# Kernel tuning notes

Measured on AMD Instinct MI355X. Metric: run time of the kernel, lower is better.

## Reference

```python
import jax, jax.numpy as jnp
import numpy as np

N = 50000        # nodes
E = 800000       # edges
H = 128          # hidden_channels
NH = 4           # num_heads
HD = H // NH     # head_dim
EPS = 1e-5       # LayerNorm eps (torch default)


def setup_inputs() -> dict:
    key = jax.random.key(0)
    ks = jax.random.split(key, 16)
    s = 0.02
    return {
        "x": jax.random.normal(ks[0], (N, H), dtype=jnp.float32),
        "edge_index": jax.random.randint(ks[1], (2, E), 0, N, dtype=jnp.int64),
        "Wq": jax.random.normal(ks[2], (H, H), dtype=jnp.float32) * s,
        "bq": jnp.zeros((H,), jnp.float32),
        "Wk": jax.random.normal(ks[3], (H, H), dtype=jnp.float32) * s,
        "bk": jnp.zeros((H,), jnp.float32),
        "Wv": jax.random.normal(ks[4], (H, H), dtype=jnp.float32) * s,
        "bv": jnp.zeros((H,), jnp.float32),
        "W1": jax.random.normal(ks[5], (2 * H, H), dtype=jnp.float32) * s,
        "b1": jnp.zeros((H,), jnp.float32),
        "ln_g": jnp.ones((H,), jnp.float32),
        "ln_b": jnp.zeros((H,), jnp.float32),
        "W2": jax.random.normal(ks[6], (H, H), dtype=jnp.float32) * s,
        "b2": jnp.zeros((H,), jnp.float32),
    }


def reference(x, edge_index, Wq, bq, Wk, bk, Wv, bv, W1, b1, ln_g, ln_b, W2, b2):
    n = x.shape[0]
    row, col = edge_index[0], edge_index[1]
    # dense projections, split heads: [N, NH, HD]
    Q = (x @ Wq + bq).reshape(n, NH, HD)
    K = (x @ Wk + bk).reshape(n, NH, HD)
    V = (x @ Wv + bv).reshape(n, NH, HD)
    # edge-wise gather + per-head dot product: [E, NH]
    scores = (Q[row] * K[col]).sum(-1) / jnp.sqrt(jnp.float32(HD))
    # segment softmax over edges grouped by destination node (row)
    m = jax.ops.segment_max(scores, row, num_segments=n)        # [N, NH]
    m = jnp.where(jnp.isfinite(m), m, 0.0)                      # empty segments -> 0
    e = jnp.exp(scores - m[row])                                # [E, NH]
    denom = jax.ops.segment_sum(e, row, num_segments=n)         # [N, NH]
    w = e / denom[row]                                          # [E, NH]
    # weighted scatter-add aggregation: [N, H]
    msg = (w[..., None] * V[col]).reshape(-1, NH * HD)          # [E, H]
    agg = jax.ops.segment_sum(msg, row, num_segments=n)         # [N, H]
    # MLP: Linear -> ReLU -> LayerNorm -> Linear, plus residual
    h = jax.nn.relu(jnp.concatenate([x, agg], axis=-1) @ W1 + b1)
    mu = h.mean(-1, keepdims=True)
    var = ((h - mu) ** 2).mean(-1, keepdims=True)
    h = (h - mu) / jnp.sqrt(var + EPS) * ln_g + ln_b
    return h @ W2 + b2 + x
```

## Files before the change

kernel.cpp:

```cpp
#include <hip/hip_runtime.h>
#include <hip/hip_bf16.h>

#define NN 50000
#define HH 128
#define NHEAD 4
#define HD 32
#define EE 800000
#define LN_EPS 1e-5f
#define ROWS_PAD 50048
#define SCAN_NB 98

typedef __bf16 bf16x8 __attribute__((ext_vector_type(8)));
typedef short  s16x8  __attribute__((ext_vector_type(8)));
typedef float  f32x4  __attribute__((ext_vector_type(4)));

__device__ __forceinline__ f32x4 mfma_bf16(s16x8 a, s16x8 b, f32x4 c) {
    return __builtin_amdgcn_mfma_f32_16x16x32_bf16((bf16x8)a, (bf16x8)b, c, 0, 0, 0);
}

__device__ __forceinline__ unsigned short f2bf(float f) {
    union { float f; unsigned int u; } v; v.f = f;
    unsigned int u = v.u + 0x7FFFu + ((v.u >> 16) & 1u);
    return (unsigned short)(u >> 16);
}
__device__ __forceinline__ float bf2f(unsigned short h) {
    union { unsigned int u; float f; } v; v.u = ((unsigned int)h) << 16;
    return v.f;
}
__device__ __forceinline__ float bflo(unsigned int w) { return __uint_as_float(w << 16); }
__device__ __forceinline__ float bfhi(unsigned int w) { return __uint_as_float(w & 0xffff0000u); }

__global__ void detect_idx_kernel(const unsigned int* __restrict__ buf, int* __restrict__ flag) {
    if (blockIdx.x == 0 && threadIdx.x == 0) {
        int is64 = 1;
        for (int i = 0; i < 64; ++i) {
            if (buf[2 * i + 1] != 0u) { is64 = 0; break; }
        }
        *flag = is64;
    }
}

__global__ void convert_hist_kernel(const void* __restrict__ ei, const int* __restrict__ flag,
                                    int* __restrict__ rowi, int* __restrict__ coli,
                                    int* __restrict__ deg) {
    int i = (blockIdx.x * blockDim.x + threadIdx.x) * 2;
    if (i >= EE) return;
    int r0, r1, c0, c1;
    if (*flag) {
        const longlong2* pr = (const longlong2*)((const long long*)ei + i);
        const longlong2* pc = (const longlong2*)((const long long*)ei + EE + i);
        longlong2 rv = *pr, cv = *pc;
        r0 = (int)rv.x; r1 = (int)rv.y;
        c0 = (int)cv.x; c1 = (int)cv.y;
    } else {
        const int2* pr = (const int2*)((const int*)ei + i);
        const int2* pc = (const int2*)((const int*)ei + EE + i);
        int2 rv = *pr, cv = *pc;
        r0 = rv.x; r1 = rv.y;
        c0 = cv.x; c1 = cv.y;
    }
    *(int2*)(rowi + i) = make_int2(r0, r1);
    *(int2*)(coli + i) = make_int2(c0, c1);
    atomicAdd(&deg[r0], 1);
    atomicAdd(&deg[r1], 1);
}

__global__ __launch_bounds__(512) void scan_a_kernel(const int* __restrict__ deg,
                                                     int* __restrict__ bsum) {
    __shared__ int red[8];
    const int t = threadIdx.x;
    const int gid = blockIdx.x * 512 + t;
    int v = (gid < NN) ? deg[gid] : 0;
    #pragma unroll
    for (int o = 1; o < 64; o <<= 1) v += __shfl_xor(v, o);
    if ((t & 63) == 0) red[t >> 6] = v;
    __syncthreads();
    if (t == 0) {
        int s = 0;
        #pragma unroll
        for (int k = 0; k < 8; ++k) s += red[k];
        bsum[blockIdx.x] = s;
    }
}

__global__ void scan_b_kernel(const int* __restrict__ bsum, int* __restrict__ boff) {
    const int lane = threadIdx.x;
    const int i0 = lane * 2, i1 = lane * 2 + 1;
    int a = (i0 < SCAN_NB) ? bsum[i0] : 0;
    int b = (i1 < SCAN_NB) ? bsum[i1] : 0;
    int incl = a + b;
    const int own = incl;
    #pragma unroll
    for (int o = 1; o < 64; o <<= 1) {
        int u = __shfl_up(incl, o);
        if (lane >= o) incl += u;
    }
    int excl = incl - own;
    if (i0 < SCAN_NB) boff[i0] = excl;
    if (i1 < SCAN_NB) boff[i1] = excl + a;
}

__global__ __launch_bounds__(512) void scan_c_kernel(const int* __restrict__ deg,
                                                     const int* __restrict__ boff,
                                                     int* __restrict__ rstart,
                                                     int* __restrict__ cursor) {
    __shared__ int wsum[8];
    const int t = threadIdx.x;
    const int gid = blockIdx.x * 512 + t;
    const int lane = t & 63, w = t >> 6;
    int v = (gid < NN) ? deg[gid] : 0;
    int incl = v;
    #pragma unroll
    for (int o = 1; o < 64; o <<= 1) {
        int u = __shfl_up(incl, o);
        if (lane >= o) incl += u;
    }
    if (lane == 63) wsum[w] = incl;
    __syncthreads();
    int woff = 0;
    for (int k = 0; k < w; ++k) woff += wsum[k];
    int excl = boff[blockIdx.x] + woff + incl - v;
    if (gid < NN) { rstart[gid] = excl; cursor[gid] = excl; }
    if (gid == 0) rstart[NN] = EE;
}

__global__ void scatter_kernel(const int* __restrict__ rowi, const int* __restrict__ coli,
                               int* __restrict__ cursor, int* __restrict__ colS) {
    int i = blockIdx.x * blockDim.x + threadIdx.x;
    if (i >= EE) return;
    int pos = atomicAdd(&cursor[rowi[i]], 1);
    colS[pos] = coli[i];
}

__global__ void pack_w_kernel(const float* __restrict__ Wq, const float* __restrict__ Wk,
                              const float* __restrict__ Wv, const float* __restrict__ W1,
                              const float* __restrict__ W2, unsigned short* __restrict__ wf) {
    int i = blockIdx.x * blockDim.x + threadIdx.x;
    if (i >= 98304) return;
    float val;
    if (i < 49152) {
        int j = i & 7, lane = (i >> 3) & 63, kk = (i >> 9) & 3, nt = i >> 11;
        int k = kk * 32 + (lane >> 4) * 8 + j;
        int n = nt * 16 + (lane & 15);
        const float* W = (n < 128) ? Wq : ((n < 256) ? Wk : Wv);
        val = W[k * HH + (n & 127)];
    } else if (i < 81920) {
        int local = i - 49152;
        int j = local & 7, lane = (local >> 3) & 63, kk = (local >> 9) & 7, nt = local >> 12;
        int k = kk * 32 + (lane >> 4) * 8 + j;
        int n = nt * 16 + (lane & 15);
        val = W1[k * HH + n];
    } else {
        int local = i - 81920;
        int j = local & 7, lane = (local >> 3) & 63, kk = (local >> 9) & 3, nt = local >> 11;
        int k = kk * 32 + (lane >> 4) * 8 + j;
        int n = nt * 16 + (lane & 15);
        val = W2[k * HH + n];
    }
    wf[i] = f2bf(val);
}

__global__ __launch_bounds__(256) void qkvx_kernel(
        const float* __restrict__ x, const unsigned short* __restrict__ wf,
        const float* __restrict__ bq, const float* __restrict__ bk, const float* __restrict__ bv,
        unsigned short* __restrict__ xa,
        unsigned short* __restrict__ Qb, unsigned short* __restrict__ Kb,
        unsigned short* __restrict__ Vb) {
    const int wave = threadIdx.x >> 6, lane = threadIdx.x & 63;
    const int row0 = blockIdx.x * 64 + wave * 16;
    const int arow = row0 + (lane & 15);
    const int kbase = (lane >> 4) * 8;

    s16x8 a[4];
    if (arow < NN) {
        const float* xp = x + (size_t)arow * HH + kbase;
        #pragma unroll
        for (int kk = 0; kk < 4; ++kk) {
            float4 f0 = *(const float4*)(xp + kk * 32);
            float4 f1 = *(const float4*)(xp + kk * 32 + 4);
            s16x8 av;
            av[0] = (short)f2bf(f0.x); av[1] = (short)f2bf(f0.y);
            av[2] = (short)f2bf(f0.z); av[3] = (short)f2bf(f0.w);
            av[4] = (short)f2bf(f1.x); av[5] = (short)f2bf(f1.y);
            av[6] = (short)f2bf(f1.z); av[7] = (short)f2bf(f1.w);
            a[kk] = av;
            *(s16x8*)(xa + (size_t)arow * 256 + kbase + kk * 32) = av;
        }
    } else {
        #pragma unroll
        for (int kk = 0; kk < 4; ++kk) a[kk] = (s16x8)0;
    }

    f32x4 acc[24];
    #pragma unroll
    for (int nt = 0; nt < 24; ++nt) acc[nt] = (f32x4){0.f, 0.f, 0.f, 0.f};

    const s16x8* wfv = (const s16x8*)wf;
    #pragma unroll
    for (int nt = 0; nt < 24; ++nt) {
        #pragma unroll
        for (int kk = 0; kk < 4; ++kk) {
            s16x8 b = wfv[(nt * 4 + kk) * 64 + lane];
            acc[nt] = mfma_bf16(a[kk], b, acc[nt]);
        }
    }

    const int colb = lane & 15;
    const int rbase = row0 + (lane >> 4) * 4;
    #pragma unroll
    for (int nt = 0; nt < 24; ++nt) {
        const int mtx = nt >> 3;
        const int nc = (nt & 7) * 16 + colb;
        const float* bias_p = (mtx == 0) ? bq : ((mtx == 1) ? bk : bv);
        unsigned short* O = (mtx == 0) ? Qb : ((mtx == 1) ? Kb : Vb);
        float bias = bias_p[nc];
        #pragma unroll
        for (int r = 0; r < 4; ++r)
            O[(size_t)(rbase + r) * 128 + nc] = f2bf(acc[nt][r] + bias);
    }
}

__global__ __launch_bounds__(256) void attn_kernel(
        const unsigned short* __restrict__ Qb, const unsigned short* __restrict__ Kb,
        const unsigned short* __restrict__ Vb, const int* __restrict__ rstart,
        const int* __restrict__ colS, unsigned short* __restrict__ xa) {
    const int wave = threadIdx.x >> 6;
    const int lane = threadIdx.x & 63;
    const int i = blockIdx.x * 4 + wave;
    if (i >= NN) return;
    const int h = lane & 3;
    const int le = lane >> 2;
    const int half = lane >> 5;
    const int sl = lane & 31;
    const int g2 = sl >> 3;
    const int e0 = rstart[i], e1 = rstart[i + 1];
    const int deg = e1 - e0;

    float qf[32];
    {
        const uint4* qp = (const uint4*)(Qb + (size_t)i * 128 + h * 32);
        #pragma unroll
        for (int cch = 0; cch < 4; ++cch) {
            uint4 qv = qp[cch];
            unsigned int w_[4] = {qv.x, qv.y, qv.z, qv.w};
            #pragma unroll
            for (int dd = 0; dd < 4; ++dd) {
                qf[cch * 8 + dd * 2]     = bflo(w_[dd]);
                qf[cch * 8 + dd * 2 + 1] = bfhi(w_[dd]);
            }
        }
    }

    float m = -INFINITY, l = 0.f;
    float acc0 = 0.f, acc1 = 0.f, acc2 = 0.f, acc3 = 0.f;

    for (int c0 = 0; c0 < deg; c0 += 16) {
        const int cnt = min(16, deg - c0);
        int col = 0;
        float s = -INFINITY;
        if (le < cnt) {
            col = colS[e0 + c0 + le];
            const uint4* kp = (const uint4*)(Kb + (size_t)col * 128 + h * 32);
            float dot = 0.f;
            #pragma unroll
            for (int cch = 0; cch < 4; ++cch) {
                uint4 kv = kp[cch];
                unsigned int w_[4] = {kv.x, kv.y, kv.z, kv.w};
                #pragma unroll
                for (int dd = 0; dd < 4; ++dd) {
                    dot += qf[cch * 8 + dd * 2]     * bflo(w_[dd]);
                    dot += qf[cch * 8 + dd * 2 + 1] * bfhi(w_[dd]);
                }
            }
            s = dot * 0.17677669529663689f;
        }
        float sm = s;
        sm = fmaxf(sm, __shfl_xor(sm, 4));
        sm = fmaxf(sm, __shfl_xor(sm, 8));
        sm = fmaxf(sm, __shfl_xor(sm, 16));
        sm = fmaxf(sm, __shfl_xor(sm, 32));
        const float mn = fmaxf(m, sm);
        const float p = (le < cnt) ? __expf(s - mn) : 0.f;
        float ps = p;
        ps += __shfl_xor(ps, 4);
        ps += __shfl_xor(ps, 8);
        ps += __shfl_xor(ps, 16);
        ps += __shfl_xor(ps, 32);
        const float fac = __expf(m - mn);
        l = l * fac + ps;
        m = mn;
        const float facbc = __shfl(fac, g2);
        acc0 *= facbc; acc1 *= facbc; acc2 *= facbc; acc3 *= facbc;
        #pragma unroll
        for (int e2 = 0; e2 < 8; ++e2) {
            const int e = 2 * e2 + half;
            const int   cbc = __shfl(col, 4 * e);
            const float pbc = __shfl(p, 4 * e + g2);
            const uint2 v2 = *(const uint2*)(Vb + (size_t)cbc * 128 + 4 * sl);
            acc0 += pbc * bflo(v2.x);
            acc1 += pbc * bfhi(v2.x);
            acc2 += pbc * bflo(v2.y);
            acc3 += pbc * bfhi(v2.y);
        }
    }

    acc0 += __shfl_xor(acc0, 32);
    acc1 += __shfl_xor(acc1, 32);
    acc2 += __shfl_xor(acc2, 32);
    acc3 += __shfl_xor(acc3, 32);
    const float lf = __shfl(l, g2);
    const float rinv = (lf > 0.f) ? 1.f / lf : 0.f;
    if (half == 0) {
        uint2 o;
        o.x = ((unsigned int)f2bf(acc1 * rinv) << 16) | (unsigned int)f2bf(acc0 * rinv);
        o.y = ((unsigned int)f2bf(acc3 * rinv) << 16) | (unsigned int)f2bf(acc2 * rinv);
        *(uint2*)(xa + (size_t)i * 256 + 128 + 4 * sl) = o;
    }
}

__global__ __launch_bounds__(256) void gemm_mlp1_kernel(
        const unsigned short* __restrict__ xa, const unsigned short* __restrict__ w1f,
        const float* __restrict__ b1, const float* __restrict__ ln_g,
        const float* __restrict__ ln_b, unsigned short* __restrict__ hb) {
    const int wave = threadIdx.x >> 6, lane = threadIdx.x & 63;
    const int row0 = blockIdx.x * 64 + wave * 16;
    const int arow = row0 + (lane & 15);

    s16x8 a[8];
    const unsigned short* ap = xa + (size_t)arow * 256 + (lane >> 4) * 8;
    #pragma unroll
    for (int kk = 0; kk < 8; ++kk) a[kk] = *(const s16x8*)(ap + kk * 32);

    f32x4 acc[8];
    #pragma unroll
    for (int nt = 0; nt < 8; ++nt) acc[nt] = (f32x4){0.f, 0.f, 0.f, 0.f};

    const s16x8* wfv = (const s16x8*)w1f;
    #pragma unroll
    for (int nt = 0; nt < 8; ++nt) {
        #pragma unroll
        for (int kk = 0; kk < 8; ++kk) {
            s16x8 b = wfv[(nt * 8 + kk) * 64 + lane];
            acc[nt] = mfma_bf16(a[kk], b, acc[nt]);
        }
    }

    const int colb = lane & 15;
    #pragma unroll
    for (int nt = 0; nt < 8; ++nt) {
        float bias = b1[nt * 16 + colb];
        #pragma unroll
        for (int r = 0; r < 4; ++r) {
            float v = acc[nt][r] + bias;
            acc[nt][r] = v > 0.f ? v : 0.f;
        }
    }
    float mu[4], rs[4];
    #pragma unroll
    for (int r = 0; r < 4; ++r) {
        float s = 0.f, q = 0.f;
        #pragma unroll
        for (int nt = 0; nt < 8; ++nt) { float v = acc[nt][r]; s += v; q += v * v; }
        #pragma unroll
        for (int msk = 1; msk < 16; msk <<= 1) {
            s += __shfl_xor(s, msk, 16);
            q += __shfl_xor(q, msk, 16);
        }
        float m_ = s * (1.f / 128.f);
        float var = q * (1.f / 128.f) - m_ * m_;
        mu[r] = m_;
        rs[r] = rsqrtf(var + LN_EPS);
    }
    const int rbase = row0 + (lane >> 4) * 4;
    #pragma unroll
    for (int nt = 0; nt < 8; ++nt) {
        int col = nt * 16 + colb;
        float g = ln_g[col], bb = ln_b[col];
        #pragma unroll
        for (int r = 0; r < 4; ++r) {
            float h = (acc[nt][r] - mu[r]) * rs[r] * g + bb;
            hb[(size_t)(rbase + r) * 128 + col] = f2bf(h);
        }
    }
}

__global__ __launch_bounds__(256) void gemm_mlp2_kernel(
        const unsigned short* __restrict__ hb, const unsigned short* __restrict__ w2f,
        const float* __restrict__ b2, const unsigned short* __restrict__ xa,
        float* __restrict__ out) {
    const int wave = threadIdx.x >> 6, lane = threadIdx.x & 63;
    const int row0 = blockIdx.x * 64 + wave * 16;
    const int arow = row0 + (lane & 15);

    s16x8 a[4];
    const unsigned short* ap = hb + (size_t)arow * 128 + (lane >> 4) * 8;
    #pragma unroll
    for (int kk = 0; kk < 4; ++kk) a[kk] = *(const s16x8*)(ap + kk * 32);

    f32x4 acc[8];
    #pragma unroll
    for (int nt = 0; nt < 8; ++nt) acc[nt] = (f32x4){0.f, 0.f, 0.f, 0.f};

    const s16x8* wfv = (const s16x8*)w2f;
    #pragma unroll
    for (int nt = 0; nt < 8; ++nt) {
        #pragma unroll
        for (int kk = 0; kk < 4; ++kk) {
            s16x8 b = wfv[(nt * 4 + kk) * 64 + lane];
            acc[nt] = mfma_bf16(a[kk], b, acc[nt]);
        }
    }

    const int colb = lane & 15;
    const int rbase = row0 + (lane >> 4) * 4;
    #pragma unroll
    for (int nt = 0; nt < 8; ++nt) {
        int col = nt * 16 + colb;
        float bias = b2[col];
        #pragma unroll
        for (int r = 0; r < 4; ++r) {
            int row = rbase + r;
            if (row < NN)
                out[(size_t)row * 128 + col] =
                    acc[nt][r] + bias + bf2f(xa[(size_t)row * 256 + col]);
        }
    }
}

extern "C" void kernel_launch(void* const* d_in, const int* in_sizes, int n_in,
                              void* d_out, int out_size, void* d_ws, size_t ws_size,
                              hipStream_t stream) {
    const float* x    = (const float*)d_in[0];
    const void*  ei   = d_in[1];
    const float* Wq   = (const float*)d_in[2];
    const float* bq   = (const float*)d_in[3];
    const float* Wk   = (const float*)d_in[4];
    const float* bk   = (const float*)d_in[5];
    const float* Wv   = (const float*)d_in[6];
    const float* bv   = (const float*)d_in[7];
    const float* W1   = (const float*)d_in[8];
    const float* b1   = (const float*)d_in[9];
    const float* ln_g = (const float*)d_in[10];
    const float* ln_b = (const float*)d_in[11];
    const float* W2   = (const float*)d_in[12];
    const float* b2   = (const float*)d_in[13];
    float* out = (float*)d_out;

    char* ws = (char*)d_ws;
    size_t off = 0;
    auto alloc = [&](size_t bytes) {
        size_t o = off;
        off = (off + bytes + 255) & ~(size_t)255;
        return o;
    };
    size_t flag_o = alloc(sizeof(int));
    size_t rowi_o = alloc((size_t)EE * sizeof(int));
    size_t coli_o = alloc((size_t)EE * sizeof(int));
    size_t deg_o  = alloc((size_t)NN * sizeof(int));
    size_t cur_o  = alloc((size_t)NN * sizeof(int));
    size_t rs_o   = alloc((size_t)(NN + 1) * sizeof(int));
    size_t bsum_o = alloc((size_t)SCAN_NB * sizeof(int));
    size_t boff_o = alloc((size_t)SCAN_NB * sizeof(int));
    size_t colS_o = alloc((size_t)EE * sizeof(int));
    size_t xa_o   = alloc((size_t)ROWS_PAD * 256 * sizeof(unsigned short));
    size_t wf_o   = alloc((size_t)98304 * sizeof(unsigned short));
    size_t Qb_o   = alloc((size_t)ROWS_PAD * 128 * sizeof(unsigned short));
    size_t Kb_o   = alloc((size_t)ROWS_PAD * 128 * sizeof(unsigned short));
    size_t Vb_o   = alloc((size_t)ROWS_PAD * 128 * sizeof(unsigned short));
    size_t hb_o   = Qb_o;

    int* flag   = (int*)(ws + flag_o);
    int* rowi   = (int*)(ws + rowi_o);
    int* coli   = (int*)(ws + coli_o);
    int* deg    = (int*)(ws + deg_o);
    int* cursor = (int*)(ws + cur_o);
    int* rstart = (int*)(ws + rs_o);
    int* bsum   = (int*)(ws + bsum_o);
    int* boff   = (int*)(ws + boff_o);
    int* colS   = (int*)(ws + colS_o);
    unsigned short* xa = (unsigned short*)(ws + xa_o);
    unsigned short* wf = (unsigned short*)(ws + wf_o);
    unsigned short* Qb = (unsigned short*)(ws + Qb_o);
    unsigned short* Kb = (unsigned short*)(ws + Kb_o);
    unsigned short* Vb = (unsigned short*)(ws + Vb_o);
    unsigned short* hb = (unsigned short*)(ws + hb_o);

    hipMemsetAsync(ws + deg_o, 0, (size_t)NN * sizeof(int), stream);

    detect_idx_kernel<<<1, 64, 0, stream>>>((const unsigned int*)ei, flag);
    convert_hist_kernel<<<(EE / 2 + 255) / 256, 256, 0, stream>>>(ei, flag, rowi, coli, deg);
    scan_a_kernel<<<SCAN_NB, 512, 0, stream>>>(deg, bsum);
    scan_b_kernel<<<1, 64, 0, stream>>>(bsum, boff);
    scan_c_kernel<<<SCAN_NB, 512, 0, stream>>>(deg, boff, rstart, cursor);
    scatter_kernel<<<(EE + 255) / 256, 256, 0, stream>>>(rowi, coli, cursor, colS);

    pack_w_kernel<<<98304 / 256, 256, 0, stream>>>(Wq, Wk, Wv, W1, W2, wf);

    qkvx_kernel<<<ROWS_PAD / 64, 256, 0, stream>>>(x, wf, bq, bk, bv, xa, Qb, Kb, Vb);

    attn_kernel<<<(NN + 3) / 4, 256, 0, stream>>>(Qb, Kb, Vb, rstart, colS, xa);

    gemm_mlp1_kernel<<<ROWS_PAD / 64, 256, 0, stream>>>(xa, wf + 49152, b1, ln_g, ln_b, hb);

    gemm_mlp2_kernel<<<ROWS_PAD / 64, 256, 0, stream>>>(hb, wf + 81920, b2, xa, out);
}
```

Before: 224.1 us.

## Build CSR via atomic ranks, fold block-offset scan, batch four nodes per attention wave

The histogram kernel now records each edge's atomic rank within its row, so the scatter writes colS at rstart[row]+rank with no second round of atomics. The rowi/coli copies and the cursor array go away, and edge_index is re-read directly. The separate block-offset scan kernel is dropped; each scan_c block sums the preceding block totals itself. The attention kernel processes four nodes per wave sequentially, which cuts the block count, but it now relies on NN being divisible by 16 and loses latency hiding from a larger grid.

Measured after the change: 193.8 us. 1.16x faster.

```diff
diff --git a/kernel.cpp b/kernel.cpp
--- a/kernel.cpp
+++ b/kernel.cpp
@@ -40,29 +40,21 @@
     }
 }
 
-__global__ void convert_hist_kernel(const void* __restrict__ ei, const int* __restrict__ flag,
-                                    int* __restrict__ rowi, int* __restrict__ coli,
-                                    int* __restrict__ deg) {
+__global__ void hist_kernel(const void* __restrict__ ei, const int* __restrict__ flag,
+                            int* __restrict__ deg, int* __restrict__ rank) {
     int i = (blockIdx.x * blockDim.x + threadIdx.x) * 2;
     if (i >= EE) return;
-    int r0, r1, c0, c1;
+    int r0, r1;
     if (*flag) {
-        const longlong2* pr = (const longlong2*)((const long long*)ei + i);
-        const longlong2* pc = (const longlong2*)((const long long*)ei + EE + i);
-        longlong2 rv = *pr, cv = *pc;
+        longlong2 rv = *(const longlong2*)((const long long*)ei + i);
         r0 = (int)rv.x; r1 = (int)rv.y;
-        c0 = (int)cv.x; c1 = (int)cv.y;
     } else {
-        const int2* pr = (const int2*)((const int*)ei + i);
-        const int2* pc = (const int2*)((const int*)ei + EE + i);
-        int2 rv = *pr, cv = *pc;
+        int2 rv = *(const int2*)((const int*)ei + i);
         r0 = rv.x; r1 = rv.y;
-        c0 = cv.x; c1 = cv.y;
-    }
-    *(int2*)(rowi + i) = make_int2(r0, r1);
-    *(int2*)(coli + i) = make_int2(c0, c1);
-    atomicAdd(&deg[r0], 1);
-    atomicAdd(&deg[r1], 1);
+    }
+    int ra = atomicAdd(&deg[r0], 1);
+    int rb = atomicAdd(&deg[r1], 1);
+    *(int2*)(rank + i) = make_int2(ra, rb);
 }
 
 __global__ __launch_bounds__(512) void scan_a_kernel(const int* __restrict__ deg,
@@ -83,31 +75,21 @@
     }
 }
 
-__global__ void scan_b_kernel(const int* __restrict__ bsum, int* __restrict__ boff) {
-    const int lane = threadIdx.x;
-    const int i0 = lane * 2, i1 = lane * 2 + 1;
-    int a = (i0 < SCAN_NB) ? bsum[i0] : 0;
-    int b = (i1 < SCAN_NB) ? bsum[i1] : 0;
-    int incl = a + b;
-    const int own = incl;
-    #pragma unroll
-    for (int o = 1; o < 64; o <<= 1) {
-        int u = __shfl_up(incl, o);
-        if (lane >= o) incl += u;
-    }
-    int excl = incl - own;
-    if (i0 < SCAN_NB) boff[i0] = excl;
-    if (i1 < SCAN_NB) boff[i1] = excl + a;
-}
-
 __global__ __launch_bounds__(512) void scan_c_kernel(const int* __restrict__ deg,
-                                                     const int* __restrict__ boff,
-                                                     int* __restrict__ rstart,
-                                                     int* __restrict__ cursor) {
+                                                     const int* __restrict__ bsum,
+                                                     int* __restrict__ rstart) {
     __shared__ int wsum[8];
+    __shared__ int blockoff;
     const int t = threadIdx.x;
     const int gid = blockIdx.x * 512 + t;
     const int lane = t & 63, w = t >> 6;
+    if (t < 64) {
+        int s = 0;
+        for (int k = t; k < blockIdx.x; k += 64) s += bsum[k];
+        #pragma unroll
+        for (int o = 1; o < 64; o <<= 1) s += __shfl_xor(s, o);
+        if (t == 0) blockoff = s;
+    }
     int v = (gid < NN) ? deg[gid] : 0;
     int incl = v;
     #pragma unroll
@@ -119,17 +101,31 @@
     __syncthreads();
     int woff = 0;
     for (int k = 0; k < w; ++k) woff += wsum[k];
-    int excl = boff[blockIdx.x] + woff + incl - v;
-    if (gid < NN) { rstart[gid] = excl; cursor[gid] = excl; }
+    int excl = blockoff + woff + incl - v;
+    if (gid < NN) rstart[gid] = excl;
     if (gid == 0) rstart[NN] = EE;
 }
 
-__global__ void scatter_kernel(const int* __restrict__ rowi, const int* __restrict__ coli,
-                               int* __restrict__ cursor, int* __restrict__ colS) {
-    int i = blockIdx.x * blockDim.x + threadIdx.x;
+__global__ void scatter_kernel(const void* __restrict__ ei, const int* __restrict__ flag,
+                               const int* __restrict__ rank, const int* __restrict__ rstart,
+                               int* __restrict__ colS) {
+    int i = (blockIdx.x * blockDim.x + threadIdx.x) * 2;
     if (i >= EE) return;
-    int pos = atomicAdd(&cursor[rowi[i]], 1);
-    colS[pos] = coli[i];
+    int r0, r1, c0, c1;
+    if (*flag) {
+        longlong2 rv = *(const longlong2*)((const long long*)ei + i);
+        longlong2 cv = *(const longlong2*)((const long long*)ei + EE + i);
+        r0 = (int)rv.x; r1 = (int)rv.y;
+        c0 = (int)cv.x; c1 = (int)cv.y;
+    } else {
+        int2 rv = *(const int2*)((const int*)ei + i);
+        int2 cv = *(const int2*)((const int*)ei + EE + i);
+        r0 = rv.x; r1 = rv.y;
+        c0 = cv.x; c1 = cv.y;
+    }
+    int2 rk = *(const int2*)(rank + i);
+    colS[rstart[r0] + rk.x] = c0;
+    colS[rstart[r1] + rk.y] = c1;
 }
 
 __global__ void pack_w_kernel(const float* __restrict__ Wq, const float* __restrict__ Wk,
@@ -226,95 +222,98 @@
         const int* __restrict__ colS, unsigned short* __restrict__ xa) {
     const int wave = threadIdx.x >> 6;
     const int lane = threadIdx.x & 63;
-    const int i = blockIdx.x * 4 + wave;
-    if (i >= NN) return;
     const int h = lane & 3;
     const int le = lane >> 2;
     const int half = lane >> 5;
     const int sl = lane & 31;
     const int g2 = sl >> 3;
-    const int e0 = rstart[i], e1 = rstart[i + 1];
-    const int deg = e1 - e0;
-
-    float qf[32];
-    {
-        const uint4* qp = (const uint4*)(Qb + (size_t)i * 128 + h * 32);
-        #pragma unroll
-        for (int cch = 0; cch < 4; ++cch) {
-            uint4 qv = qp[cch];
-            unsigned int w_[4] = {qv.x, qv.y, qv.z, qv.w};
-            #pragma unroll
-            for (int dd = 0; dd < 4; ++dd) {
-                qf[cch * 8 + dd * 2]     = bflo(w_[dd]);
-                qf[cch * 8 + dd * 2 + 1] = bfhi(w_[dd]);
-            }
-        }
-    }
-
-    float m = -INFINITY, l = 0.f;
-    float acc0 = 0.f, acc1 = 0.f, acc2 = 0.f, acc3 = 0.f;
-
-    for (int c0 = 0; c0 < deg; c0 += 16) {
-        const int cnt = min(16, deg - c0);
-        int col = 0;
-        float s = -INFINITY;
-        if (le < cnt) {
-            col = colS[e0 + c0 + le];
-            const uint4* kp = (const uint4*)(Kb + (size_t)col * 128 + h * 32);
-            float dot = 0.f;
+    const int ibase = blockIdx.x * 16 + wave * 4;
+
+    for (int j = 0; j < 4; ++j) {
+        const int i = ibase + j;
+        const int e0 = rstart[i], e1 = rstart[i + 1];
+        const int deg = e1 - e0;
+
+        float qf[32];
+        {
+            const uint4* qp = (const uint4*)(Qb + (size_t)i * 128 + h * 32);
             #pragma unroll
             for (int cch = 0; cch < 4; ++cch) {
-                uint4 kv = kp[cch];
-                unsigned int w_[4] = {kv.x, kv.y, kv.z, kv.w};
+                uint4 qv = qp[cch];
+                unsigned int w_[4] = {qv.x, qv.y, qv.z, qv.w};
                 #pragma unroll
                 for (int dd = 0; dd < 4; ++dd) {
-                    dot += qf[cch * 8 + dd * 2]     * bflo(w_[dd]);
-                    dot += qf[cch * 8 + dd * 2 + 1] * bfhi(w_[dd]);
+                    qf[cch * 8 + dd * 2]     = bflo(w_[dd]);
+                    qf[cch * 8 + dd * 2 + 1] = bfhi(w_[dd]);
                 }
             }
-            s = dot * 0.17677669529663689f;
-        }
-        float sm = s;
-        sm = fmaxf(sm, __shfl_xor(sm, 4));
-        sm = fmaxf(sm, __shfl_xor(sm, 8));
-        sm = fmaxf(sm, __shfl_xor(sm, 16));
-        sm = fmaxf(sm, __shfl_xor(sm, 32));
-        const float mn = fmaxf(m, sm);
-        const float p = (le < cnt) ? __expf(s - mn) : 0.f;
-        float ps = p;
-        ps += __shfl_xor(ps, 4);
-        ps += __shfl_xor(ps, 8);
-        ps += __shfl_xor(ps, 16);
-        ps += __shfl_xor(ps, 32);
-        const float fac = __expf(m - mn);
-        l = l * fac + ps;
-        m = mn;
-        const float facbc = __shfl(fac, g2);
-        acc0 *= facbc; acc1 *= facbc; acc2 *= facbc; acc3 *= facbc;
-        #pragma unroll
-        for (int e2 = 0; e2 < 8; ++e2) {
-            const int e = 2 * e2 + half;
-            const int   cbc = __shfl(col, 4 * e);
-            const float pbc = __shfl(p, 4 * e + g2);
-            const uint2 v2 = *(const uint2*)(Vb + (size_t)cbc * 128 + 4 * sl);
-            acc0 += pbc * bflo(v2.x);
-            acc1 += pbc * bfhi(v2.x);
-            acc2 += pbc * bflo(v2.y);
-            acc3 += pbc * bfhi(v2.y);
-        }
-    }
-
-    acc0 += __shfl_xor(acc0, 32);
-    acc1 += __shfl_xor(acc1, 32);
-    acc2 += __shfl_xor(acc2, 32);
-    acc3 += __shfl_xor(acc3, 32);
-    const float lf = __shfl(l, g2);
-    const float rinv = (lf > 0.f) ? 1.f / lf : 0.f;
-    if (half == 0) {
-        uint2 o;
-        o.x = ((unsigned int)f2bf(acc1 * rinv) << 16) | (unsigned int)f2bf(acc0 * rinv);
-        o.y = ((unsigned int)f2bf(acc3 * rinv) << 16) | (unsigned int)f2bf(acc2 * rinv);
-        *(uint2*)(xa + (size_t)i * 256 + 128 + 4 * sl) = o;
+        }
+
+        float m = -INFINITY, l = 0.f;
+        float acc0 = 0.f, acc1 = 0.f, acc2 = 0.f, acc3 = 0.f;
+
+        for (int c0 = 0; c0 < deg; c0 += 16) {
+            const int cnt = min(16, deg - c0);
+            int col = 0;
+            float s = -INFINITY;
+            if (le < cnt) {
+                col = colS[e0 + c0 + le];
+                const uint4* kp = (const uint4*)(Kb + (size_t)col * 128 + h * 32);
+                float dot = 0.f;
+                #pragma unroll
+                for (int cch = 0; cch < 4; ++cch) {
+                    uint4 kv = kp[cch];
+                    unsigned int w_[4] = {kv.x, kv.y, kv.z, kv.w};
+                    #pragma unroll
+                    for (int dd = 0; dd < 4; ++dd) {
+                        dot += qf[cch * 8 + dd * 2]     * bflo(w_[dd]);
+                        dot += qf[cch * 8 + dd * 2 + 1] * bfhi(w_[dd]);
+                    }
+                }
+                s = dot * 0.17677669529663689f;
+            }
+            float sm = s;
+            sm = fmaxf(sm, __shfl_xor(sm, 4));
+            sm = fmaxf(sm, __shfl_xor(sm, 8));
+            sm = fmaxf(sm, __shfl_xor(sm, 16));
+            sm = fmaxf(sm, __shfl_xor(sm, 32));
+            const float mn = fmaxf(m, sm);
+            const float p = (le < cnt) ? __expf(s - mn) : 0.f;
+            float ps = p;
+            ps += __shfl_xor(ps, 4);
+            ps += __shfl_xor(ps, 8);
+            ps += __shfl_xor(ps, 16);
+            ps += __shfl_xor(ps, 32);
+            const float fac = __expf(m - mn);
+            l = l * fac + ps;
+            m = mn;
+            const float facbc = __shfl(fac, g2);
+            acc0 *= facbc; acc1 *= facbc; acc2 *= facbc; acc3 *= facbc;
+            #pragma unroll
+            for (int e2 = 0; e2 < 8; ++e2) {
+                const int e = 2 * e2 + half;
+                const int   cbc = __shfl(col, 4 * e);
+                const float pbc = __shfl(p, 4 * e + g2);
+                const uint2 v2 = *(const uint2*)(Vb + (size_t)cbc * 128 + 4 * sl);
+                acc0 += pbc * bflo(v2.x);
+                acc1 += pbc * bfhi(v2.x);
+                acc2 += pbc * bflo(v2.y);
+                acc3 += pbc * bfhi(v2.y);
+            }
+        }
+
+        acc0 += __shfl_xor(acc0, 32);
+        acc1 += __shfl_xor(acc1, 32);
+        acc2 += __shfl_xor(acc2, 32);
+        acc3 += __shfl_xor(acc3, 32);
+        const float lf = __shfl(l, g2);
+        const float rinv = (lf > 0.f) ? 1.f / lf : 0.f;
+        if (half == 0) {
+            uint2 o;
+            o.x = ((unsigned int)f2bf(acc1 * rinv) << 16) | (unsigned int)f2bf(acc0 * rinv);
+            o.y = ((unsigned int)f2bf(acc3 * rinv) << 16) | (unsigned int)f2bf(acc2 * rinv);
+            *(uint2*)(xa + (size_t)i * 256 + 128 + 4 * sl) = o;
+        }
     }
 }
 
@@ -454,13 +453,10 @@
         return o;
     };
     size_t flag_o = alloc(sizeof(int));
-    size_t rowi_o = alloc((size_t)EE * sizeof(int));
-    size_t coli_o = alloc((size_t)EE * sizeof(int));
     size_t deg_o  = alloc((size_t)NN * sizeof(int));
-    size_t cur_o  = alloc((size_t)NN * sizeof(int));
+    size_t rank_o = alloc((size_t)EE * sizeof(int));
     size_t rs_o   = alloc((size_t)(NN + 1) * sizeof(int));
     size_t bsum_o = alloc((size_t)SCAN_NB * sizeof(int));
-    size_t boff_o = alloc((size_t)SCAN_NB * sizeof(int));
     size_t colS_o = alloc((size_t)EE * sizeof(int));
     size_t xa_o   = alloc((size_t)ROWS_PAD * 256 * sizeof(unsigned short));
     size_t wf_o   = alloc((size_t)98304 * sizeof(unsigned short));
@@ -470,13 +466,10 @@
     size_t hb_o   = Qb_o;
 
     int* flag   = (int*)(ws + flag_o);
-    int* rowi   = (int*)(ws + rowi_o);
-    int* coli   = (int*)(ws + coli_o);
     int* deg    = (int*)(ws + deg_o);
-    int* cursor = (int*)(ws + cur_o);
+    int* rank   = (int*)(ws + rank_o);
     int* rstart = (int*)(ws + rs_o);
     int* bsum   = (int*)(ws + bsum_o);
-    int* boff   = (int*)(ws + boff_o);
     int* colS   = (int*)(ws + colS_o);
     unsigned short* xa = (unsigned short*)(ws + xa_o);
     unsigned short* wf = (unsigned short*)(ws + wf_o);
@@ -488,17 +481,16 @@
     hipMemsetAsync(ws + deg_o, 0, (size_t)NN * sizeof(int), stream);
 
     detect_idx_kernel<<<1, 64, 0, stream>>>((const unsigned int*)ei, flag);
-    convert_hist_kernel<<<(EE / 2 + 255) / 256, 256, 0, stream>>>(ei, flag, rowi, coli, deg);
+    hist_kernel<<<(EE / 2 + 255) / 256, 256, 0, stream>>>(ei, flag, deg, rank);
     scan_a_kernel<<<SCAN_NB, 512, 0, stream>>>(deg, bsum);
-    scan_b_kernel<<<1, 64, 0, stream>>>(bsum, boff);
-    scan_c_kernel<<<SCAN_NB, 512, 0, stream>>>(deg, boff, rstart, cursor);
-    scatter_kernel<<<(EE + 255) / 256, 256, 0, stream>>>(rowi, coli, cursor, colS);
+    scan_c_kernel<<<SCAN_NB, 512, 0, stream>>>(deg, bsum, rstart);
+    scatter_kernel<<<(EE / 2 + 255) / 256, 256, 0, stream>>>(ei, flag, rank, rstart, colS);
 
     pack_w_kernel<<<98304 / 256, 256, 0, stream>>>(Wq, Wk, Wv, W1, W2, wf);
 
     qkvx_kernel<<<ROWS_PAD / 64, 256, 0, stream>>>(x, wf, bq, bk, bv, xa, Qb, Kb, Vb);
 
-    attn_kernel<<<(NN + 3) / 4, 256, 0, stream>>>(Qb, Kb, Vb, rstart, colS, xa);
+    attn_kernel<<<NN / 16, 256, 0, stream>>>(Qb, Kb, Vb, rstart, colS, xa);
 
     gemm_mlp1_kernel<<<ROWS_PAD / 64, 256, 0, stream>>>(xa, wf + 49152, b1, ln_g, ln_b, hb);
 
```
